# Kernel optimization log

Measured on AMD Instinct MI355X. Metric: run time of the kernel, lower is better.

Reference implementation:

```python
import jax, jax.numpy as jnp
import numpy as np

NUM_CLASSES = 80
ROI_SIZE = 7
SAMPLING = 2          # RoIAlign sampling_ratio
STRIDES = (4, 8, 16, 32)
FINEST_SCALE = 56.0
SCORE_THR = 0.05
IOU_THR = 0.5
MAX_PER_IMG = 100
MEANS = jnp.zeros((4,), jnp.float32)
STDS = jnp.array([0.1, 0.1, 0.2, 0.2], jnp.float32)
MAX_RATIO = abs(float(np.log(16.0 / 1000.0)))


def setup_inputs() -> dict:
    key = jax.random.key(0)
    ks = jax.random.split(key, 20)
    C, H0, W0 = 256, 200, 336
    inp = {}
    for i in range(4):
        inp[f"feat{i}"] = jax.random.normal(ks[i], (1, C, H0 >> i, W0 >> i), jnp.float32)
    N = 1000
    IMG_W, IMG_H = 1344.0, 800.0
    cx = jax.random.uniform(ks[4], (N,), minval=0.0, maxval=IMG_W)
    cy = jax.random.uniform(ks[5], (N,), minval=0.0, maxval=IMG_H)
    w = jax.random.uniform(ks[6], (N,), minval=16.0, maxval=512.0)
    h = jax.random.uniform(ks[7], (N,), minval=16.0, maxval=512.0)
    x1 = jnp.clip(cx - w / 2, 0.0, IMG_W - 1)
    y1 = jnp.clip(cy - h / 2, 0.0, IMG_H - 1)
    x2 = jnp.clip(cx + w / 2, x1 + 1.0, IMG_W)
    y2 = jnp.clip(cy + h / 2, y1 + 1.0, IMG_H)
    inp["proposals"] = jnp.stack([x1, y1, x2, y2], axis=-1)
    D = C * ROI_SIZE * ROI_SIZE  # 12544
    FC = 1024
    inp["fc1_w"] = 0.01 * jax.random.normal(ks[8], (FC, D), jnp.float32)
    inp["fc1_b"] = jnp.zeros((FC,), jnp.float32)
    inp["fc2_w"] = 0.01 * jax.random.normal(ks[9], (FC, FC), jnp.float32)
    inp["fc2_b"] = jnp.zeros((FC,), jnp.float32)
    inp["cls_w"] = 0.01 * jax.random.normal(ks[10], (NUM_CLASSES + 1, FC), jnp.float32)
    inp["cls_b"] = jnp.zeros((NUM_CLASSES + 1,), jnp.float32)
    inp["reg_w"] = 0.01 * jax.random.normal(ks[11], (NUM_CLASSES * 4, FC), jnp.float32)
    inp["reg_b"] = jnp.zeros((NUM_CLASSES * 4,), jnp.float32)
    return inp


def _roi_align(feat, rois, scale):
    # feat [C,H,W]; rois [N,4]; aligned RoIAlign, 7x7 out, sampling_ratio=2
    C, H, W = feat.shape
    P = ROI_SIZE * SAMPLING  # 14 uniform sample points per axis

    def one(roi):
        x1, y1, x2, y2 = roi[0], roi[1], roi[2], roi[3]
        sx = x1 * scale - 0.5
        sy = y1 * scale - 0.5
        rw = (x2 - x1) * scale
        rh = (y2 - y1) * scale
        pts = (jnp.arange(P, dtype=feat.dtype) + 0.5) / P
        xs = sx + pts * rw
        ys = sy + pts * rh
        y0 = jnp.floor(ys)
        x0 = jnp.floor(xs)
        ly = ys - y0
        lx = xs - x0
        y0i = jnp.clip(y0.astype(jnp.int32), 0, H - 1)
        y1i = jnp.clip(y0i + 1, 0, H - 1)
        x0i = jnp.clip(x0.astype(jnp.int32), 0, W - 1)
        x1i = jnp.clip(x0i + 1, 0, W - 1)
        g = lambda yi, xi: feat[:, yi[:, None], xi[None, :]]  # [C,P,P]
        ly_ = ly[None, :, None]
        lx_ = lx[None, None, :]
        val = (1 - ly_) * ((1 - lx_) * g(y0i, x0i) + lx_ * g(y0i, x1i)) \
            + ly_ * ((1 - lx_) * g(y1i, x0i) + lx_ * g(y1i, x1i))
        vy = ((ys >= -1.0) & (ys <= H))[None, :, None]
        vx = ((xs >= -1.0) & (xs <= W))[None, None, :]
        val = jnp.where(vy & vx, val, 0.0)
        # average-pool the 2x2 samples per bin -> [C,7,7]
        return val.reshape(C, ROI_SIZE, SAMPLING, ROI_SIZE, SAMPLING).mean(axis=(2, 4))

    return jax.vmap(one)(rois)  # [N,C,7,7]


def _delta2bbox(proposals, deltas):
    d = deltas.reshape(-1, NUM_CLASSES, 4) * STDS + MEANS
    dx, dy = d[..., 0], d[..., 1]
    dw = jnp.clip(d[..., 2], -MAX_RATIO, MAX_RATIO)
    dh = jnp.clip(d[..., 3], -MAX_RATIO, MAX_RATIO)
    px = ((proposals[:, 0] + proposals[:, 2]) * 0.5)[:, None]
    py = ((proposals[:, 1] + proposals[:, 3]) * 0.5)[:, None]
    pw = (proposals[:, 2] - proposals[:, 0])[:, None]
    ph = (proposals[:, 3] - proposals[:, 1])[:, None]
    gw = pw * jnp.exp(dw)
    gh = ph * jnp.exp(dh)
    gx = px + pw * dx
    gy = py + ph * dy
    return jnp.stack([gx - gw * 0.5, gy - gh * 0.5, gx + gw * 0.5, gy + gh * 0.5], axis=-1)


def _pairwise_iou(b):
    x1, y1, x2, y2 = b[:, 0], b[:, 1], b[:, 2], b[:, 3]
    area = jnp.maximum(x2 - x1, 0.0) * jnp.maximum(y2 - y1, 0.0)
    iw = jnp.maximum(jnp.minimum(x2[:, None], x2[None, :]) - jnp.maximum(x1[:, None], x1[None, :]), 0.0)
    ih = jnp.maximum(jnp.minimum(y2[:, None], y2[None, :]) - jnp.maximum(y1[:, None], y1[None, :]), 0.0)
    inter = iw * ih
    return inter / jnp.maximum(area[:, None] + area[None, :] - inter, 1e-8)


def _nms_one_class(boxes, scores):
    # greedy NMS, static shapes; returns score-sorted boxes/scores + keep mask
    N = scores.shape[0]
    order = jnp.argsort(-scores)
    b = boxes[order]
    s = scores[order]
    iou = _pairwise_iou(b)
    idx = jnp.arange(N)

    def body(i, keep):
        sup = (iou[i] > IOU_THR) & keep[i] & (idx > i)
        return keep & jnp.logical_not(sup)

    keep = jax.lax.fori_loop(0, N, body, s > SCORE_THR)
    return b, s, keep


def _batched_nms(bboxes, scores):
    # bboxes [N,81,4], scores [N,81]; class 80 is background (skipped)
    cls_boxes = jnp.transpose(bboxes[:, :NUM_CLASSES, :], (1, 0, 2))  # [80,N,4]
    cls_scores = scores[:, :NUM_CLASSES].T                            # [80,N]
    b, s, keep = jax.vmap(_nms_one_class)(cls_boxes, cls_scores)
    N = s.shape[1]
    s_flat = jnp.where(keep, s, -1.0).reshape(-1)
    topv, topi = jax.lax.top_k(s_flat, MAX_PER_IMG)
    det_boxes = b.reshape(-1, 4)[topi]
    det_classes = (topi // N).astype(jnp.int32)
    valid = topv > 0.0
    num_det = valid.sum().astype(jnp.int32)
    det_scores = jnp.where(valid, topv, 0.0)
    det_boxes = jnp.where(valid[:, None], det_boxes, 0.0)
    det_classes = jnp.where(valid, det_classes, -1)
    return num_det, det_boxes[None], det_scores[None], det_classes[None]


def _forward(feat0, feat1, feat2, feat3, proposals,
             fc1_w, fc1_b, fc2_w, fc2_b, cls_w, cls_b, reg_w, reg_b):
    feats = [feat0[0], feat1[0], feat2[0], feat3[0]]
    wp = proposals[:, 2] - proposals[:, 0]
    hp = proposals[:, 3] - proposals[:, 1]
    scale = jnp.sqrt(jnp.maximum(wp * hp, 1e-6))
    lvl = jnp.clip(jnp.floor(jnp.log2(scale / FINEST_SCALE + 1e-6)), 0, 3).astype(jnp.int32)
    N = proposals.shape[0]
    C = feats[0].shape[0]
    roi_feats = jnp.zeros((N, C, ROI_SIZE, ROI_SIZE), proposals.dtype)
    for l, stride in enumerate(STRIDES):
        f = _roi_align(feats[l], proposals, 1.0 / stride)
        roi_feats = jnp.where((lvl == l)[:, None, None, None], f, roi_feats)
    h = roi_feats.reshape(N, -1)
    h = jax.nn.relu(h @ fc1_w.T + fc1_b)
    h = jax.nn.relu(h @ fc2_w.T + fc2_b)
    cls_score = h @ cls_w.T + cls_b          # [N,81]
    bbox_pred = h @ reg_w.T + reg_b          # [N,320]
    scores = jax.nn.softmax(cls_score, axis=1)
    boxes = _delta2bbox(proposals, bbox_pred)                          # [N,80,4]
    boxes = jnp.concatenate([boxes, jnp.zeros((N, 1, 4), boxes.dtype)], axis=1)
    return _batched_nms(boxes, scores)


def reference(feat0, feat1, feat2, feat3, proposals,
              fc1_w, fc1_b, fc2_w, fc2_b, cls_w, cls_b, reg_w, reg_b):
    return _forward(feat0, feat1, feat2, feat3, proposals,
                    fc1_w, fc1_b, fc2_w, fc2_b, cls_w, cls_b, reg_w, reg_b)
```

## Files before the change

### kernel.cpp

```cpp
#include <hip/hip_runtime.h>
#include <math.h>

#define NCLS   80
#define NPROP  1000
#define FCDIM  1024
#define DFLAT  12544
#define MPAD   1024
#define MAXR   4.1351665567423560f
#define LDSP   40
#define NMSW   16
#define NCAT   404

#define CSPLIT 16
#define CG     (256 / CSPLIT)

typedef unsigned short ushort_t;
typedef unsigned long long ull_t;
using short8  = __attribute__((ext_vector_type(8))) short;
using float4v = __attribute__((ext_vector_type(4))) float;

__device__ inline ushort_t f2bf(float f) {
    unsigned int u = __float_as_uint(f);
    unsigned int r = (u + 0x7fffu + ((u >> 16) & 1u)) >> 16;
    return (ushort_t)r;
}

__device__ __forceinline__ unsigned cvtpk_bf16(float lo, float hi) {
    unsigned r;
    asm("v_cvt_pk_bf16_f32 %0, %1, %2" : "=v"(r) : "v"(lo), "v"(hi));
    return r;
}

__device__ __forceinline__ unsigned ordf(float f) {
    unsigned u = __float_as_uint(f);
    return (u & 0x80000000u) ? ~u : (u | 0x80000000u);
}
__device__ __forceinline__ float iordf(unsigned k) {
    unsigned u = (k & 0x80000000u) ? (k & 0x7FFFFFFFu) : ~k;
    return __uint_as_float(u);
}

__global__ __launch_bounds__(256) void roi_align_k(
    const float* __restrict__ f0, const float* __restrict__ f1,
    const float* __restrict__ f2, const float* __restrict__ f3,
    const float* __restrict__ props, ushort_t* __restrict__ Abf)
{
    int r  = blockIdx.x;
    int cz = blockIdx.y;
    int t  = threadIdx.x;

    if (r >= NPROP) {
        for (int i = t; i < CG * 49; i += 256)
            Abf[(size_t)r * DFLAT + cz * (CG * 49) + i] = 0;
        return;
    }

    const float4 p = *(const float4*)&props[(size_t)r * 4];
    float wp = p.z - p.x, hp = p.w - p.y;
    float scale = sqrtf(fmaxf(wp * hp, 1e-6f));
    int lvl = (int)floorf(log2f(scale / 56.0f + 1e-6f));
    lvl = min(max(lvl, 0), 3);

    const float* f; int H, W; float sc;
    switch (lvl) {
        case 0:  f = f0; H = 200; W = 336; sc = 0.25f;    break;
        case 1:  f = f1; H = 100; W = 168; sc = 0.125f;   break;
        case 2:  f = f2; H = 50;  W = 84;  sc = 0.0625f;  break;
        default: f = f3; H = 25;  W = 42;  sc = 0.03125f; break;
    }

    if (t >= 196) return;

    int b   = t >> 2;
    int sub = t & 3;
    int by = b / 7, bx = b - by * 7;
    int sy = by * 2 + (sub >> 1);
    int sx = bx * 2 + (sub & 1);

    float startx = p.x * sc - 0.5f, rangex = (p.z - p.x) * sc;
    float starty = p.y * sc - 0.5f, rangey = (p.w - p.y) * sc;
    float posx = startx + (((float)sx + 0.5f) / 14.0f) * rangex;
    float posy = starty + (((float)sy + 0.5f) / 14.0f) * rangey;

    float flx = floorf(posx), fly = floorf(posy);
    float lx = posx - flx, ly = posy - fly;
    int x0 = min(max((int)flx, 0), W - 1);
    int y0 = min(max((int)fly, 0), H - 1);
    int y1 = min(y0 + 1, H - 1);
    bool valid = (posx >= -1.0f) && (posx <= (float)W) &&
                 (posy >= -1.0f) && (posy <= (float)H);
    float vm = valid ? 0.25f : 0.0f;

    float w00 = (1.f - ly) * (1.f - lx) * vm;
    float w01 = (1.f - ly) * lx * vm;
    float w10 = ly * (1.f - lx) * vm;
    float w11 = ly * lx * vm;

    int  xb = min(x0, W - 2);
    bool xr = (x0 == W - 1);
    float wtA = xr ? 0.f : w00, wtB = xr ? (w00 + w01) : w01;
    float wbA = xr ? 0.f : w10, wbB = xr ? (w10 + w11) : w11;
    int ot = y0 * W + xb;
    int ob = y1 * W + xb;

    const int HW = H * W;
    ushort_t* orow = Abf + (size_t)r * DFLAT + cz * (CG * 49);
    const float* pl = f + (size_t)(cz * CG) * HW;

    #pragma unroll 8
    for (int c = 0; c < CG; c++) {
        float2 tv = *(const float2*)(pl + ot);
        float2 bv = *(const float2*)(pl + ob);
        float v = tv.x * wtA + tv.y * wtB + bv.x * wbA + bv.y * wbB;
        v += __shfl_xor(v, 1);
        v += __shfl_xor(v, 2);
        if (sub == 0)
            orow[c * 49 + b] = f2bf(v);
        pl += HW;
    }
}

__global__ __launch_bounds__(256) void gemm_sk_k(
    const ushort_t* __restrict__ A, const float* __restrict__ Wf,
    float* __restrict__ P, int N, int K, int KC)
{
    __shared__ ushort_t As[2][128 * LDSP];
    __shared__ ushort_t Bs[2][128 * LDSP];

    int tid = threadIdx.x;
    int w = tid >> 6, l = tid & 63;
    int wm = (w >> 1) * 64, wn = (w & 1) * 64;

    int bid = (int)blockIdx.x + (int)gridDim.x * ((int)blockIdx.y + (int)gridDim.y * (int)blockIdx.z);
    int bx = bid & 7;
    int slot = bid >> 3;
    int by = slot % (int)gridDim.y;
    int bz = slot / (int)gridDim.y;

    int m0 = by * 128, n0 = bx * 128;
    int kc0 = bz * KC;

    int lrow = tid >> 2;
    int lko  = (tid & 3) * 8;

    const ushort_t* Ag = A  + (size_t)(m0 + lrow) * K + kc0 + lko;
    const float*    Wg = Wf + (size_t)(n0 + lrow) * K + kc0 + lko;
    size_t rowK64 = (size_t)64 * K;

    float4v acc[4][4];
    #pragma unroll
    for (int i = 0; i < 4; i++)
        #pragma unroll
        for (int j = 0; j < 4; j++)
            acc[i][j] = (float4v){0.f, 0.f, 0.f, 0.f};

    int rl = l & 15, q = l >> 4;

    {
        uint4  a0  = *(const uint4*)(Ag);
        uint4  a1  = *(const uint4*)(Ag + rowK64);
        float4 w0a = *(const float4*)(Wg);
        float4 w0b = *(const float4*)(Wg + 4);
        float4 w1a = *(const float4*)(Wg + rowK64);
        float4 w1b = *(const float4*)(Wg + rowK64 + 4);
        uint4 wv0, wv1;
        wv0.x = cvtpk_bf16(w0a.x, w0a.y); wv0.y = cvtpk_bf16(w0a.z, w0a.w);
        wv0.z = cvtpk_bf16(w0b.x, w0b.y); wv0.w = cvtpk_bf16(w0b.z, w0b.w);
        wv1.x = cvtpk_bf16(w1a.x, w1a.y); wv1.y = cvtpk_bf16(w1a.z, w1a.w);
        wv1.z = cvtpk_bf16(w1b.x, w1b.y); wv1.w = cvtpk_bf16(w1b.z, w1b.w);
        *(uint4*)&As[0][lrow * LDSP + lko]        = a0;
        *(uint4*)&As[0][(lrow + 64) * LDSP + lko] = a1;
        *(uint4*)&Bs[0][lrow * LDSP + lko]        = wv0;
        *(uint4*)&Bs[0][(lrow + 64) * LDSP + lko] = wv1;
    }
    __syncthreads();

    int cur = 0;
    for (int k0 = 0; k0 < KC; k0 += 32) {
        bool more = (k0 + 32) < KC;

        uint4 na0, na1;
        float4 nw0a, nw0b, nw1a, nw1b;
        if (more) {
            na0  = *(const uint4*)(Ag + k0 + 32);
            na1  = *(const uint4*)(Ag + rowK64 + k0 + 32);
            nw0a = *(const float4*)(Wg + k0 + 32);
            nw0b = *(const float4*)(Wg + k0 + 36);
            nw1a = *(const float4*)(Wg + rowK64 + k0 + 32);
            nw1b = *(const float4*)(Wg + rowK64 + k0 + 36);
        }

        const ushort_t* Ac = As[cur];
        const ushort_t* Bc = Bs[cur];
        short8 af[4], bfr[4];
        #pragma unroll
        for (int i = 0; i < 4; i++)
            af[i] = *(const short8*)&Ac[(wm + i * 16 + rl) * LDSP + q * 8];
        #pragma unroll
        for (int j = 0; j < 4; j++)
            bfr[j] = *(const short8*)&Bc[(wn + j * 16 + rl) * LDSP + q * 8];

        #pragma unroll
        for (int i = 0; i < 4; i++)
            #pragma unroll
            for (int j = 0; j < 4; j++)
                acc[i][j] = __builtin_amdgcn_mfma_f32_16x16x32_bf16(
                    af[i], bfr[j], acc[i][j], 0, 0, 0);

        if (more) {
            uint4 wv0, wv1;
            wv0.x = cvtpk_bf16(nw0a.x, nw0a.y); wv0.y = cvtpk_bf16(nw0a.z, nw0a.w);
            wv0.z = cvtpk_bf16(nw0b.x, nw0b.y); wv0.w = cvtpk_bf16(nw0b.z, nw0b.w);
            wv1.x = cvtpk_bf16(nw1a.x, nw1a.y); wv1.y = cvtpk_bf16(nw1a.z, nw1a.w);
            wv1.z = cvtpk_bf16(nw1b.x, nw1b.y); wv1.w = cvtpk_bf16(nw1b.z, nw1b.w);
            ushort_t* An = As[cur ^ 1];
            ushort_t* Bn = Bs[cur ^ 1];
            *(uint4*)&An[lrow * LDSP + lko]        = na0;
            *(uint4*)&An[(lrow + 64) * LDSP + lko] = na1;
            *(uint4*)&Bn[lrow * LDSP + lko]        = wv0;
            *(uint4*)&Bn[(lrow + 64) * LDSP + lko] = wv1;
        }

        __syncthreads();
        cur ^= 1;
    }

    float* Pz = P + (size_t)bz * ((size_t)MPAD * N);
    #pragma unroll
    for (int i = 0; i < 4; i++) {
        #pragma unroll
        for (int j = 0; j < 4; j++) {
            int col = n0 + wn + j * 16 + rl;
            #pragma unroll
            for (int rr = 0; rr < 4; rr++) {
                int row = m0 + wm + i * 16 + q * 4 + rr;
                Pz[(size_t)row * N + col] = acc[i][j][rr];
            }
        }
    }
}

__global__ __launch_bounds__(256) void reduce_sk_k(
    const float* __restrict__ P, const float* __restrict__ bias,
    void* __restrict__ Cout, int N, int SK, int relu, int out_bf16)
{
    size_t idx = ((size_t)blockIdx.x * 256 + threadIdx.x) * 4;
    float4 s = *(const float4*)&P[idx];
    for (int z = 1; z < SK; z++) {
        float4 pv = *(const float4*)&P[(size_t)z * ((size_t)MPAD * N) + idx];
        s.x += pv.x; s.y += pv.y; s.z += pv.z; s.w += pv.w;
    }
    int n = (int)(idx % N);
    float4 b = *(const float4*)&bias[n];
    s.x += b.x; s.y += b.y; s.z += b.z; s.w += b.w;
    if (relu) {
        s.x = fmaxf(s.x, 0.f); s.y = fmaxf(s.y, 0.f);
        s.z = fmaxf(s.z, 0.f); s.w = fmaxf(s.w, 0.f);
    }
    if (out_bf16) {
        ushort4 o;
        o.x = f2bf(s.x); o.y = f2bf(s.y); o.z = f2bf(s.z); o.w = f2bf(s.w);
        *(ushort4*)&((ushort_t*)Cout)[idx] = o;
    } else {
        *(float4*)&((float*)Cout)[idx] = s;
    }
}

__global__ __launch_bounds__(256) void concat_w_k(
    const float* __restrict__ reg_w, const float* __restrict__ cls_w,
    const float* __restrict__ reg_b, const float* __restrict__ cls_b,
    float* __restrict__ Wcat, float* __restrict__ bcat)
{
    int row = blockIdx.x;
    int t = threadIdx.x;
    float4 v = make_float4(0.f, 0.f, 0.f, 0.f);
    float bv = 0.f;
    if (row < 320) {
        v = *(const float4*)&reg_w[(size_t)row * FCDIM + t * 4];
        bv = reg_b[row];
    } else if (row < NCAT - 3) {
        v = *(const float4*)&cls_w[(size_t)(row - 320) * FCDIM + t * 4];
        bv = cls_b[row - 320];
    }
    *(float4*)&Wcat[(size_t)row * FCDIM + t * 4] = v;
    if (t == 0) bcat[row] = bv;
}

__global__ __launch_bounds__(256) void gemm_tn_k(
    const float* __restrict__ A, const float* __restrict__ W,
    const float* __restrict__ bias, float* __restrict__ C,
    int M, int N, int K, int relu)
{
    __shared__ float As[16][64];
    __shared__ float Bs[16][64];

    int tid = threadIdx.x;
    int tx = tid & 15;
    int ty = tid >> 4;
    int m0 = blockIdx.y * 64, n0 = blockIdx.x * 64;

    int lr = tid >> 2;
    int lk = (tid & 3) << 2;

    const float* Arow = A + (size_t)(m0 + lr) * K + lk;
    const float* Wrow = W + (size_t)(n0 + lr) * K + lk;
    bool mOK = (m0 + lr) < M;
    bool nOK = (n0 + lr) < N;

    float acc[4][4] = {};

    for (int k0 = 0; k0 < K; k0 += 16) {
        float4 av = mOK ? *(const float4*)(Arow + k0) : make_float4(0.f, 0.f, 0.f, 0.f);
        float4 wv = nOK ? *(const float4*)(Wrow + k0) : make_float4(0.f, 0.f, 0.f, 0.f);
        As[lk + 0][lr] = av.x; As[lk + 1][lr] = av.y;
        As[lk + 2][lr] = av.z; As[lk + 3][lr] = av.w;
        Bs[lk + 0][lr] = wv.x; Bs[lk + 1][lr] = wv.y;
        Bs[lk + 2][lr] = wv.z; Bs[lk + 3][lr] = wv.w;
        __syncthreads();

        #pragma unroll
        for (int kk = 0; kk < 16; kk++) {
            float4 a = *(const float4*)&As[kk][ty << 2];
            float4 b = *(const float4*)&Bs[kk][tx << 2];
            acc[0][0] += a.x * b.x; acc[0][1] += a.x * b.y;
            acc[0][2] += a.x * b.z; acc[0][3] += a.x * b.w;
            acc[1][0] += a.y * b.x; acc[1][1] += a.y * b.y;
            acc[1][2] += a.y * b.z; acc[1][3] += a.y * b.w;
            acc[2][0] += a.z * b.x; acc[2][1] += a.z * b.y;
            acc[2][2] += a.z * b.z; acc[2][3] += a.z * b.w;
            acc[3][0] += a.w * b.x; acc[3][1] += a.w * b.y;
            acc[3][2] += a.w * b.z; acc[3][3] += a.w * b.w;
        }
        __syncthreads();
    }

    #pragma unroll
    for (int i = 0; i < 4; i++) {
        int m = m0 + (ty << 2) + i;
        if (m >= M) continue;
        #pragma unroll
        for (int j = 0; j < 4; j++) {
            int n = n0 + (tx << 2) + j;
            if (n < N) {
                float v = acc[i][j] + bias[n];
                if (relu) v = fmaxf(v, 0.f);
                C[(size_t)m * N + n] = v;
            }
        }
    }
}

__global__ __launch_bounds__(128) void head_post_k(
    const float* __restrict__ hr_s, const float* __restrict__ props,
    float* __restrict__ probsT, float* __restrict__ boxesT)
{
    int r = blockIdx.x, t = threadIdx.x;
    __shared__ float red[128];

    float x = (t < 81) ? hr_s[(size_t)r * NCAT + 320 + t] : -1e30f;
    red[t] = x; __syncthreads();
    for (int s = 64; s > 0; s >>= 1) {
        if (t < s) red[t] = fmaxf(red[t], red[t + s]);
        __syncthreads();
    }
    float mx = red[0];
    __syncthreads();

    float e = (t < 81) ? expf(x - mx) : 0.f;
    red[t] = e; __syncthreads();
    for (int s = 64; s > 0; s >>= 1) {
        if (t < s) red[t] += red[t + s];
        __syncthreads();
    }
    float inv = 1.f / red[0];

    if (t < NCLS) {
        probsT[(size_t)t * NPROP + r] = e * inv;

        const float4 p = *(const float4*)&props[(size_t)r * 4];
        float4 d = *(const float4*)&hr_s[(size_t)r * NCAT + t * 4];
        float dx = d.x * 0.1f, dy = d.y * 0.1f;
        float dw = fminf(fmaxf(d.z * 0.2f, -MAXR), MAXR);
        float dh = fminf(fmaxf(d.w * 0.2f, -MAXR), MAXR);
        float px = (p.x + p.z) * 0.5f, py = (p.y + p.w) * 0.5f;
        float pw = p.z - p.x, ph = p.w - p.y;
        float gw = pw * expf(dw), gh = ph * expf(dh);
        float gx = px + pw * dx, gy = py + ph * dy;
        float4 bo = make_float4(gx - gw * 0.5f, gy - gh * 0.5f,
                                gx + gw * 0.5f, gy + gh * 0.5f);
        *(float4*)&boxesT[(size_t)(t * NPROP + r) * 4] = bo;
    }
}

__global__ __launch_bounds__(512) void sort_k(
    const float* __restrict__ probsT, const float* __restrict__ boxesT,
    float* __restrict__ sortedS, float* __restrict__ sortedB)
{
    int c = blockIdx.x, t = threadIdx.x;
    __shared__ ull_t skk[1024];

    for (int j = t; j < 1024; j += 512) {
        float s = (j < NPROP) ? probsT[(size_t)c * NPROP + j] : -1e30f;
        skk[j] = ((ull_t)ordf(s) << 32) | (ull_t)(0x7FFFFFFFu - (unsigned)j);
    }
    __syncthreads();

    for (int size = 2; size <= 1024; size <<= 1) {
        for (int stride = size >> 1; stride > 0; stride >>= 1) {
            int i = (t << 1) - (t & (stride - 1));
            int j = i + stride;
            ull_t ka = skk[i], kb = skk[j];
            bool aFirst = ka > kb;
            bool desc = ((i & size) == 0);
            if (desc ? !aFirst : aFirst) {
                skk[i] = kb; skk[j] = ka;
            }
            __syncthreads();
        }
    }

    for (int j = t; j < NPROP; j += 512) {
        ull_t k = skk[j];
        int idx = (int)(0x7FFFFFFFu - (unsigned)(k & 0xFFFFFFFFull));
        sortedS[(size_t)c * NPROP + j] = iordf((unsigned)(k >> 32));
        const float4 bb = *(const float4*)&boxesT[(size_t)(c * NPROP + idx) * 4];
        *(float4*)&sortedB[(size_t)(c * NPROP + j) * 4] = bb;
    }
}

__global__ __launch_bounds__(256) void nms_k(
    const float* __restrict__ sortedS, const float* __restrict__ sortedB,
    ull_t* __restrict__ masks, float* __restrict__ candS, int* __restrict__ candI)
{
    int c = blockIdx.x, t = threadIdx.x;
    __shared__ float x1s[NPROP], y1s[NPROP], x2s[NPROP], y2s[NPROP], ars[NPROP];
    __shared__ unsigned char kp[NPROP];
    __shared__ int segc[256];

    for (int j = t; j < NPROP; j += 256) {
        float4 b = *(const float4*)&sortedB[(size_t)(c * NPROP + j) * 4];
        x1s[j] = b.x; y1s[j] = b.y; x2s[j] = b.z; y2s[j] = b.w;
        ars[j] = fmaxf(b.z - b.x, 0.f) * fmaxf(b.w - b.y, 0.f);
        kp[j] = sortedS[(size_t)c * NPROP + j] > 0.05f ? 1 : 0;
    }
    __syncthreads();

    ull_t* M = masks + (size_t)c * NPROP * NMSW;
    for (int i = t; i < NPROP; i += 256) {
        if (!kp[i]) continue;
        float xi1 = x1s[i], yi1 = y1s[i], xi2 = x2s[i], yi2 = y2s[i], ai = ars[i];
        for (int w = 0; w < NMSW; w++) {
            ull_t m = 0ull;
            int j0 = w << 6;
            #pragma unroll 4
            for (int k = 0; k < 64; k++) {
                int j = j0 + k;
                if (j < NPROP) {
                    float iw = fmaxf(fminf(xi2, x2s[j]) - fmaxf(xi1, x1s[j]), 0.f);
                    float ih = fmaxf(fminf(yi2, y2s[j]) - fmaxf(yi1, y1s[j]), 0.f);
                    float inter = iw * ih;
                    float iou = inter / fmaxf(ai + ars[j] - inter, 1e-8f);
                    if (iou > 0.5f) m |= (1ull << k);
                }
            }
            M[(size_t)i * NMSW + w] = m;
        }
    }
    __syncthreads();

    if (t < 64) {
        ull_t rem = 0ull;
        for (int i = 0; i < NPROP; i++) {
            if (kp[i]) {
                ull_t w = __shfl(rem, i >> 6);
                if ((w >> (i & 63)) & 1ull) {
                    if (t == 0) kp[i] = 0;
                } else {
                    if (t < NMSW) rem |= M[(size_t)i * NMSW + t];
                }
            }
        }
    }
    __syncthreads();

    int j0 = t * 4;
    int cnt = 0;
    #pragma unroll
    for (int k = 0; k < 4; k++) {
        int j = j0 + k;
        if (j < NPROP && kp[j]) cnt++;
    }
    segc[t] = cnt;
    __syncthreads();
    for (int off = 1; off < 256; off <<= 1) {
        int add = (t >= off) ? segc[t - off] : 0;
        __syncthreads();
        segc[t] += add;
        __syncthreads();
    }
    int pos = segc[t] - cnt;
    #pragma unroll
    for (int k = 0; k < 4; k++) {
        int j = j0 + k;
        if (j < NPROP && kp[j]) {
            if (pos < 100) {
                candS[c * 100 + pos] = sortedS[(size_t)c * NPROP + j];
                candI[c * 100 + pos] = c * NPROP + j;
            }
            pos++;
        }
    }
    int total = segc[255];
    for (int p = total + t; p < 100; p += 256) {
        candS[c * 100 + p] = -2e30f;
        candI[c * 100 + p] = 0x7fffffff;
    }
}

__global__ __launch_bounds__(256) void merge_k(
    const float* __restrict__ candS, const int* __restrict__ candI,
    const float* __restrict__ sortedB, float* __restrict__ out)
{
    int t = threadIdx.x;
    __shared__ float cs[NCLS * 101];
    __shared__ int   ci[NCLS * 101];
    __shared__ float topv[100];
    __shared__ int   topi[100];

    {
        int wv = t >> 6, ln = t & 63;
        for (int c = wv; c < NCLS; c += 4) {
            for (int j = ln; j < 100; j += 64) {
                cs[c * 101 + j] = candS[c * 100 + j];
                ci[c * 101 + j] = candI[c * 100 + j];
            }
        }
    }
    __syncthreads();

    if (t < 64) {
        int h1 = 0, h2 = 0;
        int c2 = t + 64;
        for (int r = 0; r < 100; r++) {
            float v = -2e30f; int fi = 0x7fffffff; int cls = 0;
            if (h1 < 100) { v = cs[t * 101 + h1]; fi = ci[t * 101 + h1]; cls = t; }
            if (c2 < NCLS && h2 < 100) {
                float v2 = cs[c2 * 101 + h2]; int fi2 = ci[c2 * 101 + h2];
                if (v2 > v || (v2 == v && fi2 < fi)) { v = v2; fi = fi2; cls = c2; }
            }
            #pragma unroll
            for (int s = 1; s < 64; s <<= 1) {
                float ov = __shfl_xor(v, s);
                int ofi  = __shfl_xor(fi, s);
                int ocl  = __shfl_xor(cls, s);
                if (ov > v || (ov == v && ofi < fi)) { v = ov; fi = ofi; cls = ocl; }
            }
            if (t == 0) { topv[r] = v; topi[r] = fi; }
            if (cls == t) h1++;
            else if (c2 < NCLS && cls == c2) h2++;
        }
    }
    __syncthreads();

    if (t < 100) {
        float v = topv[t]; int fi = topi[t];
        bool valid = v > 0.0f;
        float4 bb = make_float4(0.f, 0.f, 0.f, 0.f);
        if (valid) bb = *(const float4*)&sortedB[(size_t)fi * 4];
        out[1 + t * 4 + 0] = bb.x;
        out[1 + t * 4 + 1] = bb.y;
        out[1 + t * 4 + 2] = bb.z;
        out[1 + t * 4 + 3] = bb.w;
        out[401 + t] = valid ? v : 0.0f;
        out[501 + t] = valid ? (float)(fi / NPROP) : -1.0f;
    }
    if (t == 0) {
        int n = 0;
        for (int r = 0; r < 100; r++) n += (topv[r] > 0.0f) ? 1 : 0;
        out[0] = (float)n;
    }
}

extern "C" void kernel_launch(void* const* d_in, const int* in_sizes, int n_in,
                              void* d_out, int out_size, void* d_ws, size_t ws_size,
                              hipStream_t stream)
{
    const float* f0    = (const float*)d_in[0];
    const float* f1    = (const float*)d_in[1];
    const float* f2    = (const float*)d_in[2];
    const float* f3    = (const float*)d_in[3];
    const float* props = (const float*)d_in[4];
    const float* fc1_w = (const float*)d_in[5];
    const float* fc1_b = (const float*)d_in[6];
    const float* fc2_w = (const float*)d_in[7];
    const float* fc2_b = (const float*)d_in[8];
    const float* cls_w = (const float*)d_in[9];
    const float* cls_b = (const float*)d_in[10];
    const float* reg_w = (const float*)d_in[11];
    const float* reg_b = (const float*)d_in[12];
    float* out = (float*)d_out;

    unsigned char* base = (unsigned char*)d_ws;
    ushort_t* Abf  = (ushort_t*)(base);
    ushort_t* h1   = (ushort_t*)(base + 25690112);
    float*    P1   = (float*)(base + 27787264);
    float*    P2   = (float*)(base + 27787264);
    float*    h2   = (float*)(base + 44564480);
    float*    hr_s    = (float*)(base + 48758784);
    float*    probsT  = (float*)(base + 50401280);
    float*    boxesT  = (float*)(base + 50721280);
    float*    sortedS = (float*)(base + 52001280);
    float*    sortedB = (float*)(base + 52321280);
    float*    candS   = (float*)(base + 53601280);
    int*      candI   = (int*)(base + 53633280);
    float*    Wcat    = (float*)(base + 53665280);
    float*    bcat    = (float*)(base + 55320064);
    ull_t*    masks   = (ull_t*)(base);

    roi_align_k<<<dim3(MPAD, CSPLIT), 256, 0, stream>>>(f0, f1, f2, f3, props, Abf);

    gemm_sk_k<<<dim3(FCDIM / 128, MPAD / 128, 8), 256, 0, stream>>>(
        Abf, fc1_w, P1, FCDIM, DFLAT, DFLAT / 8);
    reduce_sk_k<<<(MPAD * FCDIM / 4) / 256, 256, 0, stream>>>(
        P1, fc1_b, h1, FCDIM, 8, 1, 1);

    concat_w_k<<<NCAT, 256, 0, stream>>>(reg_w, cls_w, reg_b, cls_b, Wcat, bcat);

    gemm_sk_k<<<dim3(FCDIM / 128, MPAD / 128, 4), 256, 0, stream>>>(
        h1, fc2_w, P2, FCDIM, FCDIM, FCDIM / 4);
    reduce_sk_k<<<(MPAD * FCDIM / 4) / 256, 256, 0, stream>>>(
        P2, fc2_b, h2, FCDIM, 4, 1, 0);

    gemm_tn_k<<<dim3((NCAT + 63) / 64, (NPROP + 63) / 64), 256, 0, stream>>>(
        h2, Wcat, bcat, hr_s, NPROP, NCAT, FCDIM, 0);

    head_post_k<<<NPROP, 128, 0, stream>>>(hr_s, props, probsT, boxesT);
    sort_k<<<NCLS, 512, 0, stream>>>(probsT, boxesT, sortedS, sortedB);
    nms_k<<<NCLS, 256, 0, stream>>>(sortedS, sortedB, masks, candS, candI);
    merge_k<<<1, 256, 0, stream>>>(candS, candI, sortedB, out);
}
```

Measured before the change: 546.1 us.

## Shrink split-K GEMM tile, fuse head weight concat and merge sort with NMS

The split-K bf16 GEMM tile narrows from 128x128 to 128x64, doubling the block count for the FC layers. The weight-concat kernel is removed, and the head GEMM now reads the reg/cls weights and biases directly. The sort and NMS kernels are fused into one 512-thread kernel that keeps sorted boxes and scores in shared memory, avoiding a launch and a global round trip. The smaller tile reuses each A fragment less, and the fused kernel uses more shared memory per block.

```diff
diff --git a/kernel.cpp b/kernel.cpp
--- a/kernel.cpp
+++ b/kernel.cpp
@@ -125,20 +125,14 @@
     float* __restrict__ P, int N, int K, int KC)
 {
     __shared__ ushort_t As[2][128 * LDSP];
-    __shared__ ushort_t Bs[2][128 * LDSP];
+    __shared__ ushort_t Bs[2][64 * LDSP];
 
     int tid = threadIdx.x;
     int w = tid >> 6, l = tid & 63;
-    int wm = (w >> 1) * 64, wn = (w & 1) * 64;
-
-    int bid = (int)blockIdx.x + (int)gridDim.x * ((int)blockIdx.y + (int)gridDim.y * (int)blockIdx.z);
-    int bx = bid & 7;
-    int slot = bid >> 3;
-    int by = slot % (int)gridDim.y;
-    int bz = slot / (int)gridDim.y;
-
-    int m0 = by * 128, n0 = bx * 128;
-    int kc0 = bz * KC;
+    int wm = (w >> 1) * 64, wn = (w & 1) * 32;
+
+    int m0 = blockIdx.y * 128, n0 = blockIdx.x * 64;
+    int kc0 = blockIdx.z * KC;
 
     int lrow = tid >> 2;
     int lko  = (tid & 3) * 8;
@@ -147,11 +141,11 @@
     const float*    Wg = Wf + (size_t)(n0 + lrow) * K + kc0 + lko;
     size_t rowK64 = (size_t)64 * K;
 
-    float4v acc[4][4];
+    float4v acc[4][2];
     #pragma unroll
     for (int i = 0; i < 4; i++)
         #pragma unroll
-        for (int j = 0; j < 4; j++)
+        for (int j = 0; j < 2; j++)
             acc[i][j] = (float4v){0.f, 0.f, 0.f, 0.f};
 
     int rl = l & 15, q = l >> 4;
@@ -161,17 +155,12 @@
         uint4  a1  = *(const uint4*)(Ag + rowK64);
         float4 w0a = *(const float4*)(Wg);
         float4 w0b = *(const float4*)(Wg + 4);
-        float4 w1a = *(const float4*)(Wg + rowK64);
-        float4 w1b = *(const float4*)(Wg + rowK64 + 4);
-        uint4 wv0, wv1;
+        uint4 wv0;
         wv0.x = cvtpk_bf16(w0a.x, w0a.y); wv0.y = cvtpk_bf16(w0a.z, w0a.w);
         wv0.z = cvtpk_bf16(w0b.x, w0b.y); wv0.w = cvtpk_bf16(w0b.z, w0b.w);
-        wv1.x = cvtpk_bf16(w1a.x, w1a.y); wv1.y = cvtpk_bf16(w1a.z, w1a.w);
-        wv1.z = cvtpk_bf16(w1b.x, w1b.y); wv1.w = cvtpk_bf16(w1b.z, w1b.w);
         *(uint4*)&As[0][lrow * LDSP + lko]        = a0;
         *(uint4*)&As[0][(lrow + 64) * LDSP + lko] = a1;
         *(uint4*)&Bs[0][lrow * LDSP + lko]        = wv0;
-        *(uint4*)&Bs[0][(lrow + 64) * LDSP + lko] = wv1;
     }
     __syncthreads();
 
@@ -180,56 +169,51 @@
         bool more = (k0 + 32) < KC;
 
         uint4 na0, na1;
-        float4 nw0a, nw0b, nw1a, nw1b;
+        float4 nw0a, nw0b;
         if (more) {
             na0  = *(const uint4*)(Ag + k0 + 32);
             na1  = *(const uint4*)(Ag + rowK64 + k0 + 32);
             nw0a = *(const float4*)(Wg + k0 + 32);
             nw0b = *(const float4*)(Wg + k0 + 36);
-            nw1a = *(const float4*)(Wg + rowK64 + k0 + 32);
-            nw1b = *(const float4*)(Wg + rowK64 + k0 + 36);
         }
 
         const ushort_t* Ac = As[cur];
         const ushort_t* Bc = Bs[cur];
-        short8 af[4], bfr[4];
+        short8 af[4], bfr[2];
         #pragma unroll
         for (int i = 0; i < 4; i++)
             af[i] = *(const short8*)&Ac[(wm + i * 16 + rl) * LDSP + q * 8];
         #pragma unroll
-        for (int j = 0; j < 4; j++)
+        for (int j = 0; j < 2; j++)
             bfr[j] = *(const short8*)&Bc[(wn + j * 16 + rl) * LDSP + q * 8];
 
         #pragma unroll
         for (int i = 0; i < 4; i++)
             #pragma unroll
-            for (int j = 0; j < 4; j++)
+            for (int j = 0; j < 2; j++)
                 acc[i][j] = __builtin_amdgcn_mfma_f32_16x16x32_bf16(
                     af[i], bfr[j], acc[i][j], 0, 0, 0);
 
         if (more) {
-            uint4 wv0, wv1;
+            uint4 wv0;
             wv0.x = cvtpk_bf16(nw0a.x, nw0a.y); wv0.y = cvtpk_bf16(nw0a.z, nw0a.w);
             wv0.z = cvtpk_bf16(nw0b.x, nw0b.y); wv0.w = cvtpk_bf16(nw0b.z, nw0b.w);
-            wv1.x = cvtpk_bf16(nw1a.x, nw1a.y); wv1.y = cvtpk_bf16(nw1a.z, nw1a.w);
-            wv1.z = cvtpk_bf16(nw1b.x, nw1b.y); wv1.w = cvtpk_bf16(nw1b.z, nw1b.w);
             ushort_t* An = As[cur ^ 1];
             ushort_t* Bn = Bs[cur ^ 1];
             *(uint4*)&An[lrow * LDSP + lko]        = na0;
             *(uint4*)&An[(lrow + 64) * LDSP + lko] = na1;
             *(uint4*)&Bn[lrow * LDSP + lko]        = wv0;
-            *(uint4*)&Bn[(lrow + 64) * LDSP + lko] = wv1;
         }
 
         __syncthreads();
         cur ^= 1;
     }
 
-    float* Pz = P + (size_t)bz * ((size_t)MPAD * N);
+    float* Pz = P + (size_t)blockIdx.z * ((size_t)MPAD * N);
     #pragma unroll
     for (int i = 0; i < 4; i++) {
         #pragma unroll
-        for (int j = 0; j < 4; j++) {
+        for (int j = 0; j < 2; j++) {
             int col = n0 + wn + j * 16 + rl;
             #pragma unroll
             for (int rr = 0; rr < 4; rr++) {
@@ -266,30 +250,11 @@
     }
 }
 
-__global__ __launch_bounds__(256) void concat_w_k(
+__global__ __launch_bounds__(256) void gemm_tn_k(
+    const float* __restrict__ A,
     const float* __restrict__ reg_w, const float* __restrict__ cls_w,
     const float* __restrict__ reg_b, const float* __restrict__ cls_b,
-    float* __restrict__ Wcat, float* __restrict__ bcat)
-{
-    int row = blockIdx.x;
-    int t = threadIdx.x;
-    float4 v = make_float4(0.f, 0.f, 0.f, 0.f);
-    float bv = 0.f;
-    if (row < 320) {
-        v = *(const float4*)&reg_w[(size_t)row * FCDIM + t * 4];
-        bv = reg_b[row];
-    } else if (row < NCAT - 3) {
-        v = *(const float4*)&cls_w[(size_t)(row - 320) * FCDIM + t * 4];
-        bv = cls_b[row - 320];
-    }
-    *(float4*)&Wcat[(size_t)row * FCDIM + t * 4] = v;
-    if (t == 0) bcat[row] = bv;
-}
-
-__global__ __launch_bounds__(256) void gemm_tn_k(
-    const float* __restrict__ A, const float* __restrict__ W,
-    const float* __restrict__ bias, float* __restrict__ C,
-    int M, int N, int K, int relu)
+    float* __restrict__ C, int M, int N, int K)
 {
     __shared__ float As[16][64];
     __shared__ float Bs[16][64];
@@ -303,15 +268,18 @@
     int lk = (tid & 3) << 2;
 
     const float* Arow = A + (size_t)(m0 + lr) * K + lk;
-    const float* Wrow = W + (size_t)(n0 + lr) * K + lk;
     bool mOK = (m0 + lr) < M;
-    bool nOK = (n0 + lr) < N;
+
+    int nIdx = n0 + lr;
+    const float* Wrow = nullptr;
+    if (nIdx < 320)       Wrow = reg_w + (size_t)nIdx * K + lk;
+    else if (nIdx < 401)  Wrow = cls_w + (size_t)(nIdx - 320) * K + lk;
 
     float acc[4][4] = {};
 
     for (int k0 = 0; k0 < K; k0 += 16) {
         float4 av = mOK ? *(const float4*)(Arow + k0) : make_float4(0.f, 0.f, 0.f, 0.f);
-        float4 wv = nOK ? *(const float4*)(Wrow + k0) : make_float4(0.f, 0.f, 0.f, 0.f);
+        float4 wv = Wrow ? *(const float4*)(Wrow + k0) : make_float4(0.f, 0.f, 0.f, 0.f);
         As[lk + 0][lr] = av.x; As[lk + 1][lr] = av.y;
         As[lk + 2][lr] = av.z; As[lk + 3][lr] = av.w;
         Bs[lk + 0][lr] = wv.x; Bs[lk + 1][lr] = wv.y;
@@ -342,9 +310,8 @@
         for (int j = 0; j < 4; j++) {
             int n = n0 + (tx << 2) + j;
             if (n < N) {
-                float v = acc[i][j] + bias[n];
-                if (relu) v = fmaxf(v, 0.f);
-                C[(size_t)m * N + n] = v;
+                float bb = (n < 320) ? reg_b[n] : (n < 401 ? cls_b[n - 320] : 0.f);
+                C[(size_t)m * N + n] = acc[i][j] + bb;
             }
         }
     }
@@ -392,12 +359,17 @@
     }
 }
 
-__global__ __launch_bounds__(512) void sort_k(
+__global__ __launch_bounds__(512) void sortnms_k(
     const float* __restrict__ probsT, const float* __restrict__ boxesT,
-    float* __restrict__ sortedS, float* __restrict__ sortedB)
+    float* __restrict__ sortedS, float* __restrict__ sortedB,
+    ull_t* __restrict__ masks, float* __restrict__ candS, int* __restrict__ candI)
 {
     int c = blockIdx.x, t = threadIdx.x;
     __shared__ ull_t skk[1024];
+    __shared__ float x1s[NPROP], y1s[NPROP], x2s[NPROP], y2s[NPROP], ars[NPROP];
+    __shared__ float scs[NPROP];
+    __shared__ unsigned char kp[NPROP];
+    __shared__ int segc[512];
 
     for (int j = t; j < 1024; j += 512) {
         float s = (j < NPROP) ? probsT[(size_t)c * NPROP + j] : -1e30f;
@@ -422,31 +394,19 @@
     for (int j = t; j < NPROP; j += 512) {
         ull_t k = skk[j];
         int idx = (int)(0x7FFFFFFFu - (unsigned)(k & 0xFFFFFFFFull));
-        sortedS[(size_t)c * NPROP + j] = iordf((unsigned)(k >> 32));
+        float s = iordf((unsigned)(k >> 32));
+        scs[j] = s;
+        sortedS[(size_t)c * NPROP + j] = s;
         const float4 bb = *(const float4*)&boxesT[(size_t)(c * NPROP + idx) * 4];
+        x1s[j] = bb.x; y1s[j] = bb.y; x2s[j] = bb.z; y2s[j] = bb.w;
+        ars[j] = fmaxf(bb.z - bb.x, 0.f) * fmaxf(bb.w - bb.y, 0.f);
+        kp[j] = s > 0.05f ? 1 : 0;
         *(float4*)&sortedB[(size_t)(c * NPROP + j) * 4] = bb;
     }
-}
-
-__global__ __launch_bounds__(256) void nms_k(
-    const float* __restrict__ sortedS, const float* __restrict__ sortedB,
-    ull_t* __restrict__ masks, float* __restrict__ candS, int* __restrict__ candI)
-{
-    int c = blockIdx.x, t = threadIdx.x;
-    __shared__ float x1s[NPROP], y1s[NPROP], x2s[NPROP], y2s[NPROP], ars[NPROP];
-    __shared__ unsigned char kp[NPROP];
-    __shared__ int segc[256];
-
-    for (int j = t; j < NPROP; j += 256) {
-        float4 b = *(const float4*)&sortedB[(size_t)(c * NPROP + j) * 4];
-        x1s[j] = b.x; y1s[j] = b.y; x2s[j] = b.z; y2s[j] = b.w;
-        ars[j] = fmaxf(b.z - b.x, 0.f) * fmaxf(b.w - b.y, 0.f);
-        kp[j] = sortedS[(size_t)c * NPROP + j] > 0.05f ? 1 : 0;
-    }
     __syncthreads();
 
     ull_t* M = masks + (size_t)c * NPROP * NMSW;
-    for (int i = t; i < NPROP; i += 256) {
+    for (int i = t; i < NPROP; i += 512) {
         if (!kp[i]) continue;
         float xi1 = x1s[i], yi1 = y1s[i], xi2 = x2s[i], yi2 = y2s[i], ai = ars[i];
         for (int w = 0; w < NMSW; w++) {
@@ -483,16 +443,16 @@
     }
     __syncthreads();
 
-    int j0 = t * 4;
+    int j0 = t * 2;
     int cnt = 0;
     #pragma unroll
-    for (int k = 0; k < 4; k++) {
+    for (int k = 0; k < 2; k++) {
         int j = j0 + k;
         if (j < NPROP && kp[j]) cnt++;
     }
     segc[t] = cnt;
     __syncthreads();
-    for (int off = 1; off < 256; off <<= 1) {
+    for (int off = 1; off < 512; off <<= 1) {
         int add = (t >= off) ? segc[t - off] : 0;
         __syncthreads();
         segc[t] += add;
@@ -500,18 +460,18 @@
     }
     int pos = segc[t] - cnt;
     #pragma unroll
-    for (int k = 0; k < 4; k++) {
+    for (int k = 0; k < 2; k++) {
         int j = j0 + k;
         if (j < NPROP && kp[j]) {
             if (pos < 100) {
-                candS[c * 100 + pos] = sortedS[(size_t)c * NPROP + j];
+                candS[c * 100 + pos] = scs[j];
                 candI[c * 100 + pos] = c * NPROP + j;
             }
             pos++;
         }
     }
-    int total = segc[255];
-    for (int p = total + t; p < 100; p += 256) {
+    int total = segc[511];
+    for (int p = total + t; p < 100; p += 512) {
         candS[c * 100 + p] = -2e30f;
         candI[c * 100 + p] = 0x7fffffff;
     }
@@ -613,29 +573,25 @@
     float*    sortedB = (float*)(base + 52321280);
     float*    candS   = (float*)(base + 53601280);
     int*      candI   = (int*)(base + 53633280);
-    float*    Wcat    = (float*)(base + 53665280);
-    float*    bcat    = (float*)(base + 55320064);
     ull_t*    masks   = (ull_t*)(base);
 
     roi_align_k<<<dim3(MPAD, CSPLIT), 256, 0, stream>>>(f0, f1, f2, f3, props, Abf);
 
-    gemm_sk_k<<<dim3(FCDIM / 128, MPAD / 128, 8), 256, 0, stream>>>(
+    gemm_sk_k<<<dim3(FCDIM / 64, MPAD / 128, 8), 256, 0, stream>>>(
         Abf, fc1_w, P1, FCDIM, DFLAT, DFLAT / 8);
     reduce_sk_k<<<(MPAD * FCDIM / 4) / 256, 256, 0, stream>>>(
         P1, fc1_b, h1, FCDIM, 8, 1, 1);
 
-    concat_w_k<<<NCAT, 256, 0, stream>>>(reg_w, cls_w, reg_b, cls_b, Wcat, bcat);
-
-    gemm_sk_k<<<dim3(FCDIM / 128, MPAD / 128, 4), 256, 0, stream>>>(
+    gemm_sk_k<<<dim3(FCDIM / 64, MPAD / 128, 4), 256, 0, stream>>>(
         h1, fc2_w, P2, FCDIM, FCDIM, FCDIM / 4);
     reduce_sk_k<<<(MPAD * FCDIM / 4) / 256, 256, 0, stream>>>(
         P2, fc2_b, h2, FCDIM, 4, 1, 0);
 
     gemm_tn_k<<<dim3((NCAT + 63) / 64, (NPROP + 63) / 64), 256, 0, stream>>>(
-        h2, Wcat, bcat, hr_s, NPROP, NCAT, FCDIM, 0);
+        h2, reg_w, cls_w, reg_b, cls_b, hr_s, NPROP, NCAT, FCDIM);
 
     head_post_k<<<NPROP, 128, 0, stream>>>(hr_s, props, probsT, boxesT);
-    sort_k<<<NCLS, 512, 0, stream>>>(probsT, boxesT, sortedS, sortedB);
-    nms_k<<<NCLS, 256, 0, stream>>>(sortedS, sortedB, masks, candS, candI);
+    sortnms_k<<<NCLS, 512, 0, stream>>>(probsT, boxesT, sortedS, sortedB,
+                                        masks, candS, candI);
     merge_k<<<1, 256, 0, stream>>>(candS, candI, sortedB, out);
 }
```

Result: slower. 562.9 us (+3.1%).
